# Performance work log

Measured on AMD Instinct MI355X. Metric: run time of the kernel, lower is better.

## Reference

```python
import jax, jax.numpy as jnp
import numpy as np

V, E, H, L = 50257, 1024, 1024, 52  # vocab, embed, hidden, max_length

def setup_inputs() -> dict:
    key = jax.random.key(0)
    ks = jax.random.split(key, 16)
    s = 0.02  # param init scale
    n = lambda k, shp: (jax.random.normal(k, shp, jnp.float32) * s)
    return {
        "token": jax.random.randint(ks[0], (1,), 0, V),
        "hidden": jax.random.normal(ks[1], (1, 1, H), jnp.float32),
        "encoder_outputs": jax.random.normal(ks[2], (L, H), jnp.float32),
        "emb_table": n(ks[3], (V, E)),
        "linear_w": n(ks[4], (H, E)), "linear_b": n(ks[5], (H,)),
        "attn_w": n(ks[6], (L, 2 * H)), "attn_b": n(ks[7], (L,)),
        "comb_w": n(ks[8], (H, 2 * H)), "comb_b": n(ks[9], (H,)),
        "gru_wih": n(ks[10], (3 * H, H)), "gru_whh": n(ks[11], (3 * H, H)),
        "gru_bih": n(ks[12], (3 * H,)), "gru_bhh": n(ks[13], (3 * H,)),
        "out_w": n(ks[14], (V, H)), "out_b": n(ks[15], (V,)),
    }

def reference(token, hidden, encoder_outputs, emb_table, linear_w, linear_b,
              attn_w, attn_b, comb_w, comb_b, gru_wih, gru_whh, gru_bih,
              gru_bhh, out_w, out_b):
    # embedding + linear (dropout is identity in eval mode)
    emb = emb_table[token]                                   # [1, E]
    emb = emb @ linear_w.T + linear_b                        # [1, H]
    h0 = hidden[0]                                           # [1, H]
    # Bahdanau-style attention over encoder outputs
    attn_logits = jnp.concatenate([emb, h0], axis=1) @ attn_w.T + attn_b  # [1, L]
    attn_weights = jax.nn.softmax(attn_logits, axis=-1)
    attn_applied = attn_weights @ encoder_outputs            # [1, H]
    x = jnp.concatenate([emb, attn_applied], axis=1) @ comb_w.T + comb_b  # [1, H]
    # n_layers = 1: relu then one GRU step (PyTorch GRU cell equations)
    x = jax.nn.relu(x)
    gi = x @ gru_wih.T + gru_bih                             # [1, 3H]
    gh = h0 @ gru_whh.T + gru_bhh                            # [1, 3H]
    i_r, i_z, i_n = jnp.split(gi, 3, axis=1)
    h_r, h_z, h_n = jnp.split(gh, 3, axis=1)
    r = jax.nn.sigmoid(i_r + h_r)
    z = jax.nn.sigmoid(i_z + h_z)
    n = jnp.tanh(i_n + r * h_n)
    h_new = (1.0 - z) * n + z * h0                           # [1, H]
    logits = h_new @ out_w.T + out_b                         # [1, V]
    log_probs = jax.nn.log_softmax(logits, axis=-1)
    return (log_probs, h_new[None], attn_weights)
```

## Files before the change

kernel.cpp:

```cpp
#include <hip/hip_runtime.h>
#include <hip/hip_bf16.h>
#include <stdint.h>

#define V 50257
#define E 1024
#define H 1024
#define L 52

#define NSLOT 64
#define SLOT_STRIDE 8

__device__ __forceinline__ float bf_lo(uint32_t u) { return __uint_as_float(u << 16); }
__device__ __forceinline__ float bf_hi(uint32_t u) { return __uint_as_float(u & 0xffff0000u); }

__device__ __forceinline__ float dot4(float4 a, float4 b) {
    return a.x * b.x + a.y * b.y + a.z * b.z + a.w * b.w;
}
__device__ __forceinline__ float dot8f(uint4 u, float4 a, float4 b) {
    return bf_lo(u.x) * a.x + bf_hi(u.x) * a.y + bf_lo(u.y) * a.z + bf_hi(u.y) * a.w +
           bf_lo(u.z) * b.x + bf_hi(u.z) * b.y + bf_lo(u.w) * b.z + bf_hi(u.w) * b.w;
}
__device__ __forceinline__ float dot8bb(uint4 u, uint4 v) {
    return bf_lo(u.x) * bf_lo(v.x) + bf_hi(u.x) * bf_hi(v.x) +
           bf_lo(u.y) * bf_lo(v.y) + bf_hi(u.y) * bf_hi(v.y) +
           bf_lo(u.z) * bf_lo(v.z) + bf_hi(u.z) * bf_hi(v.z) +
           bf_lo(u.w) * bf_lo(v.w) + bf_hi(u.w) * bf_hi(v.w);
}

__device__ __forceinline__ float wred(float v) {
#pragma unroll
    for (int o = 32; o; o >>= 1) v += __shfl_down(v, o, 64);
    return v;
}

__device__ __forceinline__ int detect_f32(const void* probe) {
    uint32_t u = ((const uint32_t*)probe)[threadIdx.x & 63];
    float lo = __uint_as_float(u << 16);
    int bad = (lo != lo) || (fabsf(lo) > 100.f);
    unsigned long long m = __ballot(bad);
    return (__popcll(m) > 4) ? 1 : 0;
}

__global__ __launch_bounds__(256) void k_emb_attn0(const int* __restrict__ token,
                                                   const void* __restrict__ embt,
                                                   const void* __restrict__ linw,
                                                   const void* __restrict__ linb,
                                                   const void* __restrict__ attw,
                                                   const void* __restrict__ attb,
                                                   const void* __restrict__ h0,
                                                   float* __restrict__ emb_lin,
                                                   float* __restrict__ attn_lg0,
                                                   float* __restrict__ S_parts) {
    const int lane = threadIdx.x & 63, wid = threadIdx.x >> 6;
    const int isf32 = detect_f32(embt);
    if (blockIdx.x == 0 && threadIdx.x < NSLOT) S_parts[threadIdx.x * SLOT_STRIDE] = 0.f;

    if (blockIdx.x < 256) {
        const int h = blockIdx.x * 4 + wid;
        float acc = 0.f, bias;
        if (isf32) {
            const float4* e = (const float4*)((const float*)embt + (size_t)token[0] * E);
            const float4* w = (const float4*)((const float*)linw + (size_t)h * E);
#pragma unroll
            for (int k = lane; k < 256; k += 64) acc += dot4(w[k], e[k]);
            bias = ((const float*)linb)[h];
        } else {
            const uint4* e = (const uint4*)((const __hip_bfloat16*)embt + (size_t)token[0] * E);
            const uint4* w = (const uint4*)((const __hip_bfloat16*)linw + (size_t)h * E);
#pragma unroll
            for (int k = lane; k < 128; k += 64) acc += dot8bb(w[k], e[k]);
            bias = __bfloat162float(((const __hip_bfloat16*)linb)[h]);
        }
        acc = wred(acc);
        if (lane == 0) emb_lin[h] = acc + bias;
    } else {
        const int l = (blockIdx.x - 256) * 4 + wid;
        float acc = 0.f, bias;
        if (isf32) {
            const float4* w = (const float4*)((const float*)attw + (size_t)l * 2 * H + H);
            const float4* h0f = (const float4*)(const float*)h0;
#pragma unroll
            for (int k = lane; k < 256; k += 64) acc += dot4(w[k], h0f[k]);
            bias = ((const float*)attb)[l];
        } else {
            const uint4* w = (const uint4*)((const __hip_bfloat16*)attw + (size_t)l * 2 * H + H);
            const uint4* h0u = (const uint4*)(const __hip_bfloat16*)h0;
#pragma unroll
            for (int k = lane; k < 128; k += 64) acc += dot8bb(w[k], h0u[k]);
            bias = __bfloat162float(((const __hip_bfloat16*)attb)[l]);
        }
        acc = wred(acc);
        if (lane == 0) attn_lg0[l] = acc + bias;
    }
}

__global__ __launch_bounds__(1024) void k_attn(const float* __restrict__ emb_lin,
                                               const float* __restrict__ attn_lg0,
                                               const void* __restrict__ attw,
                                               const void* __restrict__ enc,
                                               const void* __restrict__ probe,
                                               float* __restrict__ attn_app,
                                               float* __restrict__ out_attn) {
    __shared__ float lg[L];
    __shared__ float aw[L];
    const int tid = threadIdx.x, lane = tid & 63, wid = tid >> 6;
    const int isf32 = detect_f32(probe);
    const float4* ef = (const float4*)emb_lin;
    for (int l = wid; l < L; l += 16) {
        float acc = 0.f;
        if (isf32) {
            const float4* w = (const float4*)((const float*)attw + (size_t)l * 2 * H);
#pragma unroll
            for (int k = lane; k < 256; k += 64) acc += dot4(w[k], ef[k]);
        } else {
            const uint4* w = (const uint4*)((const __hip_bfloat16*)attw + (size_t)l * 2 * H);
#pragma unroll
            for (int k = lane; k < 128; k += 64) acc += dot8f(w[k], ef[2 * k], ef[2 * k + 1]);
        }
        acc = wred(acc);
        if (lane == 0) lg[l] = acc + attn_lg0[l];
    }
    __syncthreads();
    if (tid < 64) {
        float x = (tid < L) ? lg[tid] : -1e30f;
        float m = x;
#pragma unroll
        for (int o = 32; o; o >>= 1) m = fmaxf(m, __shfl_down(m, o, 64));
        m = __shfl(m, 0, 64);
        float e = (tid < L) ? expf(x - m) : 0.f;
        float s = e;
#pragma unroll
        for (int o = 32; o; o >>= 1) s += __shfl_down(s, o, 64);
        s = __shfl(s, 0, 64);
        if (tid < L) aw[tid] = e / s;
    }
    __syncthreads();
    if (tid < L) out_attn[tid] = aw[tid];
    float acc = 0.f;
    if (isf32) {
        const float* e = (const float*)enc;
        for (int l = 0; l < L; l++) acc += aw[l] * e[l * H + tid];
    } else {
        const __hip_bfloat16* e = (const __hip_bfloat16*)enc;
        for (int l = 0; l < L; l++) acc += aw[l] * __bfloat162float(e[l * H + tid]);
    }
    attn_app[tid] = acc;
}

__global__ __launch_bounds__(256) void k_comb(const float* __restrict__ cat2,
                                              const void* __restrict__ combw,
                                              const void* __restrict__ combb,
                                              const void* __restrict__ probe,
                                              float* __restrict__ xvec) {
    const int lane = threadIdx.x & 63, wid = threadIdx.x >> 6;
    const int h = blockIdx.x * 4 + wid;
    const int isf32 = detect_f32(probe);
    const float4* cf = (const float4*)cat2;
    float acc = 0.f, bias;
    if (isf32) {
        const float4* w = (const float4*)((const float*)combw + (size_t)h * 2 * H);
#pragma unroll
        for (int k = lane; k < 512; k += 64) acc += dot4(w[k], cf[k]);
        bias = ((const float*)combb)[h];
    } else {
        const uint4* w = (const uint4*)((const __hip_bfloat16*)combw + (size_t)h * 2 * H);
#pragma unroll
        for (int k = lane; k < 256; k += 64) acc += dot8f(w[k], cf[2 * k], cf[2 * k + 1]);
        bias = __bfloat162float(((const __hip_bfloat16*)combb)[h]);
    }
    acc = wred(acc);
    if (lane == 0) xvec[h] = fmaxf(acc + bias, 0.f);
}

__global__ __launch_bounds__(256) void k_gru(const float* __restrict__ xvec,
                                             const void* __restrict__ h0,
                                             const void* __restrict__ wih,
                                             const void* __restrict__ whh,
                                             const void* __restrict__ bih,
                                             const void* __restrict__ bhh,
                                             const void* __restrict__ probe,
                                             float* __restrict__ hnew,
                                             float* __restrict__ out_h) {
    const int lane = threadIdx.x & 63, wid = threadIdx.x >> 6;
    const int j = blockIdx.x * 4 + wid;
    const int isf32 = detect_f32(probe);
    const float4* xf = (const float4*)xvec;
    float a0 = 0, a1 = 0, a2 = 0, b0 = 0, b1 = 0, b2 = 0;
    float bi0, bi1, bi2, bh0, bh1, bh2, h0j;
    if (isf32) {
        const float* wi = (const float*)wih;
        const float* wh = (const float*)whh;
        const float4* wi0 = (const float4*)(wi + (size_t)j * H);
        const float4* wi1 = (const float4*)(wi + (size_t)(j + H) * H);
        const float4* wi2 = (const float4*)(wi + (size_t)(j + 2 * H) * H);
        const float4* wh0 = (const float4*)(wh + (size_t)j * H);
        const float4* wh1 = (const float4*)(wh + (size_t)(j + H) * H);
        const float4* wh2 = (const float4*)(wh + (size_t)(j + 2 * H) * H);
        const float4* h0f = (const float4*)(const float*)h0;
#pragma unroll
        for (int k = lane; k < 256; k += 64) {
            float4 xa = xf[k];
            a0 += dot4(wi0[k], xa); a1 += dot4(wi1[k], xa); a2 += dot4(wi2[k], xa);
            float4 hv = h0f[k];
            b0 += dot4(wh0[k], hv); b1 += dot4(wh1[k], hv); b2 += dot4(wh2[k], hv);
        }
        bi0 = ((const float*)bih)[j]; bi1 = ((const float*)bih)[j + H]; bi2 = ((const float*)bih)[j + 2 * H];
        bh0 = ((const float*)bhh)[j]; bh1 = ((const float*)bhh)[j + H]; bh2 = ((const float*)bhh)[j + 2 * H];
        h0j = ((const float*)h0)[j];
    } else {
        const __hip_bfloat16* wi = (const __hip_bfloat16*)wih;
        const __hip_bfloat16* wh = (const __hip_bfloat16*)whh;
        const uint4* wi0 = (const uint4*)(wi + (size_t)j * H);
        const uint4* wi1 = (const uint4*)(wi + (size_t)(j + H) * H);
        const uint4* wi2 = (const uint4*)(wi + (size_t)(j + 2 * H) * H);
        const uint4* wh0 = (const uint4*)(wh + (size_t)j * H);
        const uint4* wh1 = (const uint4*)(wh + (size_t)(j + H) * H);
        const uint4* wh2 = (const uint4*)(wh + (size_t)(j + 2 * H) * H);
        const uint4* h0u = (const uint4*)(const __hip_bfloat16*)h0;
#pragma unroll
        for (int k = lane; k < 128; k += 64) {
            float4 xa = xf[2 * k], xb = xf[2 * k + 1];
            a0 += dot8f(wi0[k], xa, xb); a1 += dot8f(wi1[k], xa, xb); a2 += dot8f(wi2[k], xa, xb);
            uint4 hv = h0u[k];
            b0 += dot8bb(wh0[k], hv); b1 += dot8bb(wh1[k], hv); b2 += dot8bb(wh2[k], hv);
        }
        const __hip_bfloat16* bi = (const __hip_bfloat16*)bih;
        const __hip_bfloat16* bh = (const __hip_bfloat16*)bhh;
        bi0 = __bfloat162float(bi[j]); bi1 = __bfloat162float(bi[j + H]); bi2 = __bfloat162float(bi[j + 2 * H]);
        bh0 = __bfloat162float(bh[j]); bh1 = __bfloat162float(bh[j + H]); bh2 = __bfloat162float(bh[j + 2 * H]);
        h0j = __bfloat162float(((const __hip_bfloat16*)h0)[j]);
    }
    a0 = wred(a0); a1 = wred(a1); a2 = wred(a2);
    b0 = wred(b0); b1 = wred(b1); b2 = wred(b2);
    if (lane == 0) {
        float r = 1.f / (1.f + expf(-((a0 + bi0) + (b0 + bh0))));
        float z = 1.f / (1.f + expf(-((a1 + bi1) + (b1 + bh1))));
        float n = tanhf((a2 + bi2) + r * (b2 + bh2));
        float hj = (1.f - z) * n + z * h0j;
        hnew[j] = hj;
        out_h[j] = hj;
    }
}

__global__ __launch_bounds__(256) void k_logits(const float* __restrict__ hnew,
                                                const void* __restrict__ outw,
                                                const void* __restrict__ outb,
                                                const void* __restrict__ probe,
                                                float* __restrict__ out,
                                                float* __restrict__ S_parts) {
    const int lane = threadIdx.x & 63, wid = threadIdx.x >> 6;
    const int v = blockIdx.x * 4 + wid;
    const int isf32 = detect_f32(probe);
    __shared__ float part[4];
    float acc = 0.f, bias = 0.f;
    if (v < V) {
        if (isf32) {
            const float4* w = (const float4*)((const float*)outw + (size_t)v * H);
            const float4* hf = (const float4*)hnew;
#pragma unroll
            for (int k = lane; k < 256; k += 64) acc += dot4(w[k], hf[k]);
            bias = ((const float*)outb)[v];
        } else {
            const uint4* w = (const uint4*)((const __hip_bfloat16*)outw + (size_t)v * H);
            const float4* hf = (const float4*)hnew;
#pragma unroll
            for (int k = lane; k < 128; k += 64) acc += dot8f(w[k], hf[2 * k], hf[2 * k + 1]);
            bias = __bfloat162float(((const __hip_bfloat16*)outb)[v]);
        }
    }
    acc = wred(acc);
    if (lane == 0) {
        float e = 0.f;
        if (v < V) {
            float val = acc + bias;
            out[v] = val;
            e = expf(val);
        }
        part[wid] = e;
    }
    __syncthreads();
    if (threadIdx.x == 0)
        atomicAdd(&S_parts[(blockIdx.x & (NSLOT - 1)) * SLOT_STRIDE],
                  part[0] + part[1] + part[2] + part[3]);
}

__global__ __launch_bounds__(256) void k_final(const float* __restrict__ S_parts,
                                               float* __restrict__ out) {
    __shared__ float lsS;
    const int tid = threadIdx.x;
    if (tid < 64) {
        float s = S_parts[tid * SLOT_STRIDE];
#pragma unroll
        for (int o = 32; o; o >>= 1) s += __shfl_down(s, o, 64);
        if (tid == 0) lsS = logf(s);
    }
    __syncthreads();
    const int v = blockIdx.x * 256 + tid;
    if (v < V) out[v] -= lsS;
}

extern "C" void kernel_launch(void* const* d_in, const int* in_sizes, int n_in,
                              void* d_out, int out_size, void* d_ws, size_t ws_size,
                              hipStream_t stream) {
    const int* token = (const int*)d_in[0];
    const void* hidden = d_in[1];
    const void* enc = d_in[2];
    const void* embt = d_in[3];
    const void* linw = d_in[4];
    const void* linb = d_in[5];
    const void* attw = d_in[6];
    const void* attb = d_in[7];
    const void* combw = d_in[8];
    const void* combb = d_in[9];
    const void* wih = d_in[10];
    const void* whh = d_in[11];
    const void* bih = d_in[12];
    const void* bhh = d_in[13];
    const void* outw = d_in[14];
    const void* outb = d_in[15];
    float* out = (float*)d_out;

    float* ws = (float*)d_ws;
    float* S_parts = ws;
    float* emb_lin = ws + 512;
    float* attn_app = ws + 512 + 1024;
    float* xvec = ws + 512 + 2048;
    float* hnew = ws + 512 + 3072;
    float* attn_lg0 = ws + 512 + 4096;
    float* cat2 = emb_lin;

    k_emb_attn0<<<269, 256, 0, stream>>>(token, embt, linw, linb, attw, attb, hidden,
                                         emb_lin, attn_lg0, S_parts);
    k_attn<<<1, 1024, 0, stream>>>(emb_lin, attn_lg0, attw, enc, embt, attn_app,
                                   out + (V + H));
    k_comb<<<256, 256, 0, stream>>>(cat2, combw, combb, embt, xvec);
    k_gru<<<256, 256, 0, stream>>>(xvec, hidden, wih, whh, bih, bhh, embt, hnew, out + V);
    k_logits<<<(V + 3) / 4, 256, 0, stream>>>(hnew, outw, outb, embt, out, S_parts);
    k_final<<<(V + 255) / 256, 256, 0, stream>>>(S_parts, out);
}
```

Measured before the change: 428.6 us.

## Fuse decoder pipeline into one cooperative persistent kernel with grid syncs

```diff
diff --git a/kernel.cpp b/kernel.cpp
--- a/kernel.cpp
+++ b/kernel.cpp
@@ -1,11 +1,18 @@
 #include <hip/hip_runtime.h>
 #include <hip/hip_bf16.h>
+#include <hip/hip_cooperative_groups.h>
 #include <stdint.h>
+
+namespace cg = cooperative_groups;
 
 #define V 50257
 #define E 1024
 #define H 1024
 #define L 52
+
+#define NB 256
+#define NT 512
+#define NWAVE 2048
 
 #define NSLOT 64
 #define SLOT_STRIDE 8
@@ -39,6 +46,290 @@
     int bad = (lo != lo) || (fabsf(lo) > 100.f);
     unsigned long long m = __ballot(bad);
     return (__popcll(m) > 4) ? 1 : 0;
+}
+
+__global__ __launch_bounds__(NT) void k_mega(
+    const int* __restrict__ token, const void* __restrict__ h0,
+    const void* __restrict__ enc, const void* __restrict__ embt,
+    const void* __restrict__ linw, const void* __restrict__ linb,
+    const void* __restrict__ attw, const void* __restrict__ attb,
+    const void* __restrict__ combw, const void* __restrict__ combb,
+    const void* __restrict__ wih, const void* __restrict__ whh,
+    const void* __restrict__ bih, const void* __restrict__ bhh,
+    const void* __restrict__ outw, const void* __restrict__ outb,
+    float* __restrict__ out, float* __restrict__ ws) {
+    cg::grid_group grid = cg::this_grid();
+    const int tid = threadIdx.x, lane = tid & 63, wid = tid >> 6;
+    const int gw = (int)blockIdx.x * (NT / 64) + wid;
+    const int isf32 = detect_f32(embt);
+
+    float* emb_lin = ws;
+    float* attn_app = ws + 1024;
+    float* attn_lg0 = ws + 2048;
+    float* xvec = ws + 2112;
+    float* hnew = ws + 3136;
+    float* S_parts = ws + 4160;
+    float* ghs = ws + 4416;
+
+    __shared__ float s_lg[L], s_aw[L], s_part[NT / 64];
+
+    if (gw < 1024) {
+        const int h = gw;
+        float acc = 0.f, bias;
+        if (isf32) {
+            const float4* e = (const float4*)((const float*)embt + (size_t)token[0] * E);
+            const float4* w = (const float4*)((const float*)linw + (size_t)h * E);
+#pragma unroll
+            for (int k = lane; k < 256; k += 64) acc += dot4(w[k], e[k]);
+            bias = ((const float*)linb)[h];
+        } else {
+            const uint4* e = (const uint4*)((const __hip_bfloat16*)embt + (size_t)token[0] * E);
+            const uint4* w = (const uint4*)((const __hip_bfloat16*)linw + (size_t)h * E);
+#pragma unroll
+            for (int k = lane; k < 128; k += 64) acc += dot8bb(w[k], e[k]);
+            bias = __bfloat162float(((const __hip_bfloat16*)linb)[h]);
+        }
+        acc = wred(acc);
+        if (lane == 0) emb_lin[h] = acc + bias;
+        if (gw < L) {
+            const int l = gw;
+            float acc2 = 0.f, bias2;
+            if (isf32) {
+                const float4* w = (const float4*)((const float*)attw + (size_t)l * 2 * H + H);
+                const float4* h0f = (const float4*)(const float*)h0;
+#pragma unroll
+                for (int k = lane; k < 256; k += 64) acc2 += dot4(w[k], h0f[k]);
+                bias2 = ((const float*)attb)[l];
+            } else {
+                const uint4* w = (const uint4*)((const __hip_bfloat16*)attw + (size_t)l * 2 * H + H);
+                const uint4* h0u = (const uint4*)(const __hip_bfloat16*)h0;
+#pragma unroll
+                for (int k = lane; k < 128; k += 64) acc2 += dot8bb(w[k], h0u[k]);
+                bias2 = __bfloat162float(((const __hip_bfloat16*)attb)[l]);
+            }
+            acc2 = wred(acc2);
+            if (lane == 0) attn_lg0[l] = acc2 + bias2;
+        }
+    } else {
+        const int j = gw - 1024;
+        float b0 = 0, b1 = 0, b2 = 0;
+        if (isf32) {
+            const float* wh = (const float*)whh;
+            const float4* wh0 = (const float4*)(wh + (size_t)j * H);
+            const float4* wh1 = (const float4*)(wh + (size_t)(j + H) * H);
+            const float4* wh2 = (const float4*)(wh + (size_t)(j + 2 * H) * H);
+            const float4* h0f = (const float4*)(const float*)h0;
+#pragma unroll
+            for (int k = lane; k < 256; k += 64) {
+                float4 hv = h0f[k];
+                b0 += dot4(wh0[k], hv); b1 += dot4(wh1[k], hv); b2 += dot4(wh2[k], hv);
+            }
+        } else {
+            const __hip_bfloat16* wh = (const __hip_bfloat16*)whh;
+            const uint4* wh0 = (const uint4*)(wh + (size_t)j * H);
+            const uint4* wh1 = (const uint4*)(wh + (size_t)(j + H) * H);
+            const uint4* wh2 = (const uint4*)(wh + (size_t)(j + 2 * H) * H);
+            const uint4* h0u = (const uint4*)(const __hip_bfloat16*)h0;
+#pragma unroll
+            for (int k = lane; k < 128; k += 64) {
+                uint4 hv = h0u[k];
+                b0 += dot8bb(wh0[k], hv); b1 += dot8bb(wh1[k], hv); b2 += dot8bb(wh2[k], hv);
+            }
+        }
+        b0 = wred(b0); b1 = wred(b1); b2 = wred(b2);
+        if (lane == 0) { ghs[j] = b0; ghs[j + 1024] = b1; ghs[j + 2048] = b2; }
+    }
+    grid.sync();
+
+    if (blockIdx.x == 0) {
+        const float4* ef = (const float4*)emb_lin;
+        for (int l = wid; l < L; l += NT / 64) {
+            float acc = 0.f;
+            if (isf32) {
+                const float4* w = (const float4*)((const float*)attw + (size_t)l * 2 * H);
+#pragma unroll
+                for (int k = lane; k < 256; k += 64) acc += dot4(w[k], ef[k]);
+            } else {
+                const uint4* w = (const uint4*)((const __hip_bfloat16*)attw + (size_t)l * 2 * H);
+#pragma unroll
+                for (int k = lane; k < 128; k += 64) acc += dot8f(w[k], ef[2 * k], ef[2 * k + 1]);
+            }
+            acc = wred(acc);
+            if (lane == 0) s_lg[l] = acc + attn_lg0[l];
+        }
+        __syncthreads();
+        if (tid < 64) {
+            float x = (tid < L) ? s_lg[tid] : -1e30f;
+            float m = x;
+#pragma unroll
+            for (int o = 32; o; o >>= 1) m = fmaxf(m, __shfl_down(m, o, 64));
+            m = __shfl(m, 0, 64);
+            float e = (tid < L) ? expf(x - m) : 0.f;
+            float s = e;
+#pragma unroll
+            for (int o = 32; o; o >>= 1) s += __shfl_down(s, o, 64);
+            s = __shfl(s, 0, 64);
+            if (tid < L) s_aw[tid] = e / s;
+        }
+        __syncthreads();
+        if (tid < L) out[(size_t)V + H + tid] = s_aw[tid];
+        for (int h = tid; h < H; h += NT) {
+            float acc = 0.f;
+            if (isf32) {
+                const float* e = (const float*)enc;
+                for (int l = 0; l < L; l++) acc += s_aw[l] * e[l * H + h];
+            } else {
+                const __hip_bfloat16* e = (const __hip_bfloat16*)enc;
+                for (int l = 0; l < L; l++) acc += s_aw[l] * __bfloat162float(e[l * H + h]);
+            }
+            attn_app[h] = acc;
+        }
+    }
+    grid.sync();
+
+    if (gw < 1024) {
+        const int h = gw;
+        const float4* cf = (const float4*)ws;
+        float acc = 0.f, bias;
+        if (isf32) {
+            const float4* w = (const float4*)((const float*)combw + (size_t)h * 2 * H);
+#pragma unroll
+            for (int k = lane; k < 512; k += 64) acc += dot4(w[k], cf[k]);
+            bias = ((const float*)combb)[h];
+        } else {
+            const uint4* w = (const uint4*)((const __hip_bfloat16*)combw + (size_t)h * 2 * H);
+#pragma unroll
+            for (int k = lane; k < 256; k += 64) acc += dot8f(w[k], cf[2 * k], cf[2 * k + 1]);
+            bias = __bfloat162float(((const __hip_bfloat16*)combb)[h]);
+        }
+        acc = wred(acc);
+        if (lane == 0) xvec[h] = fmaxf(acc + bias, 0.f);
+    }
+    grid.sync();
+
+    if (gw < 1024) {
+        const int j = gw;
+        const float4* xf = (const float4*)xvec;
+        float a0 = 0, a1 = 0, a2 = 0;
+        if (isf32) {
+            const float* wi = (const float*)wih;
+            const float4* wi0 = (const float4*)(wi + (size_t)j * H);
+            const float4* wi1 = (const float4*)(wi + (size_t)(j + H) * H);
+            const float4* wi2 = (const float4*)(wi + (size_t)(j + 2 * H) * H);
+#pragma unroll
+            for (int k = lane; k < 256; k += 64) {
+                float4 xa = xf[k];
+                a0 += dot4(wi0[k], xa); a1 += dot4(wi1[k], xa); a2 += dot4(wi2[k], xa);
+            }
+        } else {
+            const __hip_bfloat16* wi = (const __hip_bfloat16*)wih;
+            const uint4* wi0 = (const uint4*)(wi + (size_t)j * H);
+            const uint4* wi1 = (const uint4*)(wi + (size_t)(j + H) * H);
+            const uint4* wi2 = (const uint4*)(wi + (size_t)(j + 2 * H) * H);
+#pragma unroll
+            for (int k = lane; k < 128; k += 64) {
+                float4 xa = xf[2 * k], xb = xf[2 * k + 1];
+                a0 += dot8f(wi0[k], xa, xb); a1 += dot8f(wi1[k], xa, xb); a2 += dot8f(wi2[k], xa, xb);
+            }
+        }
+        a0 = wred(a0); a1 = wred(a1); a2 = wred(a2);
+        if (lane == 0) {
+            float bi0, bi1, bi2, bh0, bh1, bh2, h0j;
+            if (isf32) {
+                bi0 = ((const float*)bih)[j]; bi1 = ((const float*)bih)[j + H]; bi2 = ((const float*)bih)[j + 2 * H];
+                bh0 = ((const float*)bhh)[j]; bh1 = ((const float*)bhh)[j + H]; bh2 = ((const float*)bhh)[j + 2 * H];
+                h0j = ((const float*)h0)[j];
+            } else {
+                const __hip_bfloat16* bi = (const __hip_bfloat16*)bih;
+                const __hip_bfloat16* bh = (const __hip_bfloat16*)bhh;
+                bi0 = __bfloat162float(bi[j]); bi1 = __bfloat162float(bi[j + H]); bi2 = __bfloat162float(bi[j + 2 * H]);
+                bh0 = __bfloat162float(bh[j]); bh1 = __bfloat162float(bh[j + H]); bh2 = __bfloat162float(bh[j + 2 * H]);
+                h0j = __bfloat162float(((const __hip_bfloat16*)h0)[j]);
+            }
+            float b0 = ghs[j], b1 = ghs[j + 1024], b2 = ghs[j + 2048];
+            float r = 1.f / (1.f + expf(-((a0 + bi0) + (b0 + bh0))));
+            float z = 1.f / (1.f + expf(-((a1 + bi1) + (b1 + bh1))));
+            float n = tanhf((a2 + bi2) + r * (b2 + bh2));
+            float hj = (1.f - z) * n + z * h0j;
+            hnew[j] = hj;
+            out[(size_t)V + j] = hj;
+        }
+    }
+    grid.sync();
+
+    float sumexp = 0.f;
+    if (isf32) {
+        const float4* hf = (const float4*)hnew;
+        float4 h0v = hf[lane], h1v = hf[lane + 64], h2v = hf[lane + 128], h3v = hf[lane + 192];
+        const float* W = (const float*)outw;
+        const float* B = (const float*)outb;
+        for (int v = gw; v < V; v += 2 * NWAVE) {
+            const int v2 = v + NWAVE;
+            const float4* w1 = (const float4*)(W + (size_t)v * H);
+            float acc1 = dot4(w1[lane], h0v) + dot4(w1[lane + 64], h1v) +
+                         dot4(w1[lane + 128], h2v) + dot4(w1[lane + 192], h3v);
+            float acc2 = 0.f;
+            if (v2 < V) {
+                const float4* w2 = (const float4*)(W + (size_t)v2 * H);
+                acc2 = dot4(w2[lane], h0v) + dot4(w2[lane + 64], h1v) +
+                       dot4(w2[lane + 128], h2v) + dot4(w2[lane + 192], h3v);
+            }
+            acc1 = wred(acc1); acc2 = wred(acc2);
+            if (lane == 0) {
+                float val = acc1 + B[v];
+                out[v] = val;
+                sumexp += expf(val);
+                if (v2 < V) {
+                    float val2 = acc2 + B[v2];
+                    out[v2] = val2;
+                    sumexp += expf(val2);
+                }
+            }
+        }
+    } else {
+        const float4* hf = (const float4*)hnew;
+        float4 ha0 = hf[2 * lane], hb0 = hf[2 * lane + 1];
+        float4 ha1 = hf[2 * (lane + 64)], hb1 = hf[2 * (lane + 64) + 1];
+        const __hip_bfloat16* W = (const __hip_bfloat16*)outw;
+        const __hip_bfloat16* B = (const __hip_bfloat16*)outb;
+        for (int v = gw; v < V; v += 2 * NWAVE) {
+            const int v2 = v + NWAVE;
+            const uint4* w1 = (const uint4*)(W + (size_t)v * H);
+            float acc1 = dot8f(w1[lane], ha0, hb0) + dot8f(w1[lane + 64], ha1, hb1);
+            float acc2 = 0.f;
+            if (v2 < V) {
+                const uint4* w2 = (const uint4*)(W + (size_t)v2 * H);
+                acc2 = dot8f(w2[lane], ha0, hb0) + dot8f(w2[lane + 64], ha1, hb1);
+            }
+            acc1 = wred(acc1); acc2 = wred(acc2);
+            if (lane == 0) {
+                float val = acc1 + __bfloat162float(B[v]);
+                out[v] = val;
+                sumexp += expf(val);
+                if (v2 < V) {
+                    float val2 = acc2 + __bfloat162float(B[v2]);
+                    out[v2] = val2;
+                    sumexp += expf(val2);
+                }
+            }
+        }
+    }
+    if (lane == 0) s_part[wid] = sumexp;
+    __syncthreads();
+    if (tid == 0) {
+        float s = 0.f;
+#pragma unroll
+        for (int i = 0; i < NT / 64; i++) s += s_part[i];
+        S_parts[blockIdx.x] = s;
+    }
+    grid.sync();
+
+    float s = S_parts[lane] + S_parts[lane + 64] + S_parts[lane + 128] + S_parts[lane + 192];
+    s = wred(s);
+    s = __shfl(s, 0, 64);
+    float logS = logf(s);
+    const int v = (int)blockIdx.x * NT + tid;
+    if (v < V) out[v] -= logS;
 }
 
 __global__ __launch_bounds__(256) void k_emb_attn0(const int* __restrict__ token,
@@ -319,14 +610,23 @@
     const void* outw = d_in[14];
     const void* outb = d_in[15];
     float* out = (float*)d_out;
-
-    float* ws = (float*)d_ws;
-    float* S_parts = ws;
-    float* emb_lin = ws + 512;
-    float* attn_app = ws + 512 + 1024;
-    float* xvec = ws + 512 + 2048;
-    float* hnew = ws + 512 + 3072;
-    float* attn_lg0 = ws + 512 + 4096;
+    float* wsf = (float*)d_ws;
+
+    void* args[] = {(void*)&token, (void*)&hidden, (void*)&enc, (void*)&embt,
+                    (void*)&linw, (void*)&linb, (void*)&attw, (void*)&attb,
+                    (void*)&combw, (void*)&combb, (void*)&wih, (void*)&whh,
+                    (void*)&bih, (void*)&bhh, (void*)&outw, (void*)&outb,
+                    (void*)&out, (void*)&wsf};
+    hipError_t err = hipLaunchCooperativeKernel((void*)k_mega, dim3(NB), dim3(NT),
+                                                args, 0, stream);
+    if (err == hipSuccess) return;
+
+    float* S_parts = wsf;
+    float* emb_lin = wsf + 512;
+    float* attn_app = wsf + 512 + 1024;
+    float* xvec = wsf + 512 + 2048;
+    float* hnew = wsf + 512 + 3072;
+    float* attn_lg0 = wsf + 512 + 4096;
     float* cat2 = emb_lin;
 
     k_emb_attn0<<<269, 256, 0, stream>>>(token, embt, linw, linb, attw, attb, hidden,
```

Measured after the change: 608.1 us. 41.9% more time.

## Hoist GRU hidden-to-hidden matvec into the front kernel

Applied to the files above, without the earlier changes.

```diff
diff --git a/kernel.cpp b/kernel.cpp
--- a/kernel.cpp
+++ b/kernel.cpp
@@ -41,22 +41,25 @@
     return (__popcll(m) > 4) ? 1 : 0;
 }
 
-__global__ __launch_bounds__(256) void k_emb_attn0(const int* __restrict__ token,
-                                                   const void* __restrict__ embt,
-                                                   const void* __restrict__ linw,
-                                                   const void* __restrict__ linb,
-                                                   const void* __restrict__ attw,
-                                                   const void* __restrict__ attb,
-                                                   const void* __restrict__ h0,
-                                                   float* __restrict__ emb_lin,
-                                                   float* __restrict__ attn_lg0,
-                                                   float* __restrict__ S_parts) {
+__global__ __launch_bounds__(256) void k_front(const int* __restrict__ token,
+                                               const void* __restrict__ embt,
+                                               const void* __restrict__ linw,
+                                               const void* __restrict__ linb,
+                                               const void* __restrict__ attw,
+                                               const void* __restrict__ attb,
+                                               const void* __restrict__ whh,
+                                               const void* __restrict__ h0,
+                                               float* __restrict__ emb_lin,
+                                               float* __restrict__ attn_lg0,
+                                               float* __restrict__ ghs,
+                                               float* __restrict__ S_parts) {
     const int lane = threadIdx.x & 63, wid = threadIdx.x >> 6;
+    const int b = blockIdx.x;
     const int isf32 = detect_f32(embt);
-    if (blockIdx.x == 0 && threadIdx.x < NSLOT) S_parts[threadIdx.x * SLOT_STRIDE] = 0.f;
-
-    if (blockIdx.x < 256) {
-        const int h = blockIdx.x * 4 + wid;
+    if (b == 0 && threadIdx.x < NSLOT) S_parts[threadIdx.x * SLOT_STRIDE] = 0.f;
+
+    if (b < 256) {
+        const int h = b * 4 + wid;
         float acc = 0.f, bias;
         if (isf32) {
             const float4* e = (const float4*)((const float*)embt + (size_t)token[0] * E);
@@ -73,8 +76,8 @@
         }
         acc = wred(acc);
         if (lane == 0) emb_lin[h] = acc + bias;
-    } else {
-        const int l = (blockIdx.x - 256) * 4 + wid;
+    } else if (b < 269) {
+        const int l = (b - 256) * 4 + wid;
         float acc = 0.f, bias;
         if (isf32) {
             const float4* w = (const float4*)((const float*)attw + (size_t)l * 2 * H + H);
@@ -91,6 +94,22 @@
         }
         acc = wred(acc);
         if (lane == 0) attn_lg0[l] = acc + bias;
+    } else {
+        const int r = (b - 269) * 4 + wid;
+        float acc = 0.f;
+        if (isf32) {
+            const float4* w = (const float4*)((const float*)whh + (size_t)r * H);
+            const float4* h0f = (const float4*)(const float*)h0;
+#pragma unroll
+            for (int k = lane; k < 256; k += 64) acc += dot4(w[k], h0f[k]);
+        } else {
+            const uint4* w = (const uint4*)((const __hip_bfloat16*)whh + (size_t)r * H);
+            const uint4* h0u = (const uint4*)(const __hip_bfloat16*)h0;
+#pragma unroll
+            for (int k = lane; k < 128; k += 64) acc += dot8bb(w[k], h0u[k]);
+        }
+        acc = wred(acc);
+        if (lane == 0) ghs[r] = acc;
     }
 }
 
@@ -175,9 +194,9 @@
 __global__ __launch_bounds__(256) void k_gru(const float* __restrict__ xvec,
                                              const void* __restrict__ h0,
                                              const void* __restrict__ wih,
-                                             const void* __restrict__ whh,
                                              const void* __restrict__ bih,
                                              const void* __restrict__ bhh,
+                                             const float* __restrict__ ghs,
                                              const void* __restrict__ probe,
                                              float* __restrict__ hnew,
                                              float* __restrict__ out_h) {
@@ -185,54 +204,43 @@
     const int j = blockIdx.x * 4 + wid;
     const int isf32 = detect_f32(probe);
     const float4* xf = (const float4*)xvec;
-    float a0 = 0, a1 = 0, a2 = 0, b0 = 0, b1 = 0, b2 = 0;
-    float bi0, bi1, bi2, bh0, bh1, bh2, h0j;
+    float a0 = 0, a1 = 0, a2 = 0;
     if (isf32) {
         const float* wi = (const float*)wih;
-        const float* wh = (const float*)whh;
         const float4* wi0 = (const float4*)(wi + (size_t)j * H);
         const float4* wi1 = (const float4*)(wi + (size_t)(j + H) * H);
         const float4* wi2 = (const float4*)(wi + (size_t)(j + 2 * H) * H);
-        const float4* wh0 = (const float4*)(wh + (size_t)j * H);
-        const float4* wh1 = (const float4*)(wh + (size_t)(j + H) * H);
-        const float4* wh2 = (const float4*)(wh + (size_t)(j + 2 * H) * H);
-        const float4* h0f = (const float4*)(const float*)h0;
 #pragma unroll
         for (int k = lane; k < 256; k += 64) {
             float4 xa = xf[k];
             a0 += dot4(wi0[k], xa); a1 += dot4(wi1[k], xa); a2 += dot4(wi2[k], xa);
-            float4 hv = h0f[k];
-            b0 += dot4(wh0[k], hv); b1 += dot4(wh1[k], hv); b2 += dot4(wh2[k], hv);
-        }
-        bi0 = ((const float*)bih)[j]; bi1 = ((const float*)bih)[j + H]; bi2 = ((const float*)bih)[j + 2 * H];
-        bh0 = ((const float*)bhh)[j]; bh1 = ((const float*)bhh)[j + H]; bh2 = ((const float*)bhh)[j + 2 * H];
-        h0j = ((const float*)h0)[j];
+        }
     } else {
         const __hip_bfloat16* wi = (const __hip_bfloat16*)wih;
-        const __hip_bfloat16* wh = (const __hip_bfloat16*)whh;
         const uint4* wi0 = (const uint4*)(wi + (size_t)j * H);
         const uint4* wi1 = (const uint4*)(wi + (size_t)(j + H) * H);
         const uint4* wi2 = (const uint4*)(wi + (size_t)(j + 2 * H) * H);
-        const uint4* wh0 = (const uint4*)(wh + (size_t)j * H);
-        const uint4* wh1 = (const uint4*)(wh + (size_t)(j + H) * H);
-        const uint4* wh2 = (const uint4*)(wh + (size_t)(j + 2 * H) * H);
-        const uint4* h0u = (const uint4*)(const __hip_bfloat16*)h0;
 #pragma unroll
         for (int k = lane; k < 128; k += 64) {
             float4 xa = xf[2 * k], xb = xf[2 * k + 1];
             a0 += dot8f(wi0[k], xa, xb); a1 += dot8f(wi1[k], xa, xb); a2 += dot8f(wi2[k], xa, xb);
-            uint4 hv = h0u[k];
-            b0 += dot8bb(wh0[k], hv); b1 += dot8bb(wh1[k], hv); b2 += dot8bb(wh2[k], hv);
-        }
-        const __hip_bfloat16* bi = (const __hip_bfloat16*)bih;
-        const __hip_bfloat16* bh = (const __hip_bfloat16*)bhh;
-        bi0 = __bfloat162float(bi[j]); bi1 = __bfloat162float(bi[j + H]); bi2 = __bfloat162float(bi[j + 2 * H]);
-        bh0 = __bfloat162float(bh[j]); bh1 = __bfloat162float(bh[j + H]); bh2 = __bfloat162float(bh[j + 2 * H]);
-        h0j = __bfloat162float(((const __hip_bfloat16*)h0)[j]);
+        }
     }
     a0 = wred(a0); a1 = wred(a1); a2 = wred(a2);
-    b0 = wred(b0); b1 = wred(b1); b2 = wred(b2);
     if (lane == 0) {
+        float bi0, bi1, bi2, bh0, bh1, bh2, h0j;
+        if (isf32) {
+            bi0 = ((const float*)bih)[j]; bi1 = ((const float*)bih)[j + H]; bi2 = ((const float*)bih)[j + 2 * H];
+            bh0 = ((const float*)bhh)[j]; bh1 = ((const float*)bhh)[j + H]; bh2 = ((const float*)bhh)[j + 2 * H];
+            h0j = ((const float*)h0)[j];
+        } else {
+            const __hip_bfloat16* bi = (const __hip_bfloat16*)bih;
+            const __hip_bfloat16* bh = (const __hip_bfloat16*)bhh;
+            bi0 = __bfloat162float(bi[j]); bi1 = __bfloat162float(bi[j + H]); bi2 = __bfloat162float(bi[j + 2 * H]);
+            bh0 = __bfloat162float(bh[j]); bh1 = __bfloat162float(bh[j + H]); bh2 = __bfloat162float(bh[j + 2 * H]);
+            h0j = __bfloat162float(((const __hip_bfloat16*)h0)[j]);
+        }
+        float b0 = ghs[j], b1 = ghs[j + 1024], b2 = ghs[j + 2048];
         float r = 1.f / (1.f + expf(-((a0 + bi0) + (b0 + bh0))));
         float z = 1.f / (1.f + expf(-((a1 + bi1) + (b1 + bh1))));
         float n = tanhf((a2 + bi2) + r * (b2 + bh2));
@@ -327,14 +335,15 @@
     float* xvec = ws + 512 + 2048;
     float* hnew = ws + 512 + 3072;
     float* attn_lg0 = ws + 512 + 4096;
+    float* ghs = ws + 512 + 4160;
     float* cat2 = emb_lin;
 
-    k_emb_attn0<<<269, 256, 0, stream>>>(token, embt, linw, linb, attw, attb, hidden,
-                                         emb_lin, attn_lg0, S_parts);
+    k_front<<<1037, 256, 0, stream>>>(token, embt, linw, linb, attw, attb, whh, hidden,
+                                      emb_lin, attn_lg0, ghs, S_parts);
     k_attn<<<1, 1024, 0, stream>>>(emb_lin, attn_lg0, attw, enc, embt, attn_app,
                                    out + (V + H));
     k_comb<<<256, 256, 0, stream>>>(cat2, combw, combb, embt, xvec);
-    k_gru<<<256, 256, 0, stream>>>(xvec, hidden, wih, whh, bih, bhh, embt, hnew, out + V);
+    k_gru<<<256, 256, 0, stream>>>(xvec, hidden, wih, bih, bhh, ghs, embt, hnew, out + V);
     k_logits<<<(V + 3) / 4, 256, 0, stream>>>(hnew, outw, outb, embt, out, S_parts);
     k_final<<<(V + 255) / 256, 256, 0, stream>>>(S_parts, out);
 }
```

Measured after the change: 426.8 us. No clear change (-0.4%).
